# Performance work log

Hardware: AMD Instinct MI355X
Metric: run time of the kernel (lower is better)

## Reference

```python
import jax, jax.numpy as jnp
import numpy as np

N_EMBED = 2048
NUM_EXPERTS = 64
TOP_K = 8
B, S = 4, 8192


def setup_inputs() -> dict:
    key = jax.random.key(0)
    ks = jax.random.split(key, 8)
    scale = 1.0 / np.sqrt(N_EMBED)
    return {
        "x": jax.random.normal(ks[0], (B, S, N_EMBED), dtype=jnp.float32),
        "eps": jax.random.normal(ks[1], (B, S, NUM_EXPERTS), dtype=jnp.float32),
        "w_router": jax.random.uniform(ks[2], (N_EMBED, NUM_EXPERTS), jnp.float32, -scale, scale),
        "b_router": jax.random.uniform(ks[3], (NUM_EXPERTS,), jnp.float32, -scale, scale),
        "w_noise": jax.random.uniform(ks[4], (N_EMBED, NUM_EXPERTS), jnp.float32, -scale, scale),
        "b_noise": jax.random.uniform(ks[5], (NUM_EXPERTS,), jnp.float32, -scale, scale),
        "w_skip": jax.random.uniform(ks[6], (N_EMBED, 1), jnp.float32, -scale, scale),
        "b_skip": jax.random.uniform(ks[7], (1,), jnp.float32, -scale, scale),
    }


def reference(x, eps, w_router, b_router, w_noise, b_noise, w_skip, b_skip):
    # Router and noise logits: [B, S, E]
    logits = jnp.einsum("bsd,de->bse", x, w_router) + b_router
    noise_logits = jnp.einsum("bsd,de->bse", x, w_noise) + b_noise
    # noisy_logits = logits + randn * softplus(noise_logits); randn passed as eps
    noisy_logits = logits + eps * jax.nn.softplus(noise_logits)
    # top-k + scatter(-inf) + softmax == softmax over top-k values scattered back
    top_vals, indices = jax.lax.top_k(noisy_logits, TOP_K)  # [B,S,K]
    gates = jax.nn.softmax(top_vals, axis=-1)  # [B,S,K]
    onehot = jax.nn.one_hot(indices, NUM_EXPERTS, dtype=x.dtype)  # [B,S,K,E]
    router_output = jnp.einsum("bsk,bske->bse", gates, onehot)  # zeros off top-k
    # Sigmoid skip gate: [B, S, 1]
    skip_prob = jax.nn.sigmoid(jnp.einsum("bsd,do->bso", x, w_skip) + b_skip)
    return router_output, indices, skip_prob
```

## Files before the change

kernel.cpp:

```cpp
#include <hip/hip_runtime.h>
#include <math.h>

#define NTOK   32768
#define D      2048
#define E      64
#define TOPK   8

#define BLOCK  256
#define TM     64
#define BK     32
#define NCHUNK (D / BK)
#define NBLK   (NTOK / TM)

#define WBF_BYTES (NCHUNK * 16384)

#define LG_STR 133
#define SP_OFF  34048
#define SMEM_BYTES 34304

#define TIE_EPS 2e-4f

typedef __bf16 bf16x8 __attribute__((ext_vector_type(8)));
typedef float  f32x4  __attribute__((ext_vector_type(4)));

__device__ __forceinline__ unsigned short f2bf_rne(float f) {
    unsigned int u = __float_as_uint(f);
    u += 0x7FFFu + ((u >> 16) & 1u);
    return (unsigned short)(u >> 16);
}

__device__ __forceinline__ void split_pack8(const float* xv, uint4& hv, uint4& lv) {
    unsigned int h[8], l[8];
#pragma unroll
    for (int j = 0; j < 8; ++j) {
        unsigned short hb = f2bf_rne(xv[j]);
        float hf = __uint_as_float(((unsigned int)hb) << 16);
        unsigned short lb = f2bf_rne(xv[j] - hf);
        h[j] = hb; l[j] = lb;
    }
    hv.x = h[0] | (h[1] << 16); hv.y = h[2] | (h[3] << 16);
    hv.z = h[4] | (h[5] << 16); hv.w = h[6] | (h[7] << 16);
    lv.x = l[0] | (l[1] << 16); lv.y = l[2] | (l[3] << 16);
    lv.z = l[4] | (l[5] << 16); lv.w = l[6] | (l[7] << 16);
}

__global__ __launch_bounds__(256) void convert_w_kernel(
    const float* __restrict__ wr, const float* __restrict__ wn, char* __restrict__ wbf)
{
    int u = blockIdx.x * 256 + threadIdx.x;
    int col  = u & 127;
    int koct = (u >> 7) & 3;
    int c    = u >> 9;
    const float* src = (col < 64)
        ? (wr + (size_t)(c * BK + koct * 8) * E + col)
        : (wn + (size_t)(c * BK + koct * 8) * E + (col - 64));
    float xv[8];
#pragma unroll
    for (int j = 0; j < 8; ++j) xv[j] = src[(size_t)j * E];
    uint4 hv, lv;
    split_pack8(xv, hv, lv);
    char* dst = wbf + (size_t)c * 16384 + (size_t)(koct * 128 + col) * 16;
    *(uint4*)dst = hv;
    *(uint4*)(dst + 8192) = lv;
}

__global__ __launch_bounds__(BLOCK, 2) void router_kernel(
    const float* __restrict__ x, const float* __restrict__ eps,
    const char* __restrict__ wbf,
    const float* __restrict__ b_router, const float* __restrict__ b_noise,
    const float* __restrict__ w_skip, const float* __restrict__ b_skip,
    float* __restrict__ out_router, float* __restrict__ out_idx,
    float* __restrict__ out_skip, int* __restrict__ flags, int cap)
{
    __shared__ __attribute__((aligned(16))) char smem[SMEM_BYTES];
    const int tid = threadIdx.x;
    const int tokBase = blockIdx.x * TM;

    const int lane = tid & 63;
    const int wv   = __builtin_amdgcn_readfirstlane(tid >> 6);
    const int tg   = wv >> 1;
    const int ch   = wv & 1;
    const int q    = lane >> 4;
    const int m    = lane & 15;

    const float* xlane = x + (size_t)(tokBase + tg * 32 + m) * D + q * 8;
    const char*  blane = wbf + (size_t)((q << 7) + (ch << 6) + m) * 16;
    const float* wklane = w_skip + q * 8;

    f32x4 acc[2][4];
#pragma unroll
    for (int tt = 0; tt < 2; ++tt)
#pragma unroll
        for (int cw = 0; cw < 4; ++cw) acc[tt][cw] = (f32x4){0.f, 0.f, 0.f, 0.f};
    float skipAcc[2] = {0.f, 0.f};

    struct Gen {
        float4 a[2][2];
        uint4  b[4][2];
        float4 wk[2];
    };

    auto loadGen = [&](Gen& g, int c) {
        const float* xp = xlane + c * BK;
#pragma unroll
        for (int tt = 0; tt < 2; ++tt) {
            g.a[tt][0] = *(const float4*)(xp + (size_t)tt * 16 * D);
            g.a[tt][1] = *(const float4*)(xp + (size_t)tt * 16 * D + 4);
        }
        const char* bp = blane + (size_t)c * 16384;
#pragma unroll
        for (int cw = 0; cw < 4; ++cw) {
            g.b[cw][0] = *(const uint4*)(bp + cw * 256);
            g.b[cw][1] = *(const uint4*)(bp + cw * 256 + 8192);
        }
        g.wk[0] = *(const float4*)(wklane + c * BK);
        g.wk[1] = *(const float4*)(wklane + c * BK + 4);
    };

    auto computeGen = [&](Gen& g) {
#pragma unroll
        for (int tt = 0; tt < 2; ++tt) {
            float xv[8] = {g.a[tt][0].x, g.a[tt][0].y, g.a[tt][0].z, g.a[tt][0].w,
                           g.a[tt][1].x, g.a[tt][1].y, g.a[tt][1].z, g.a[tt][1].w};
            uint4 hv, lv;
            split_pack8(xv, hv, lv);
            bf16x8 Ah = __builtin_bit_cast(bf16x8, hv);
            bf16x8 Al = __builtin_bit_cast(bf16x8, lv);
#pragma unroll
            for (int cw = 0; cw < 4; ++cw) {
                bf16x8 Bh = __builtin_bit_cast(bf16x8, g.b[cw][0]);
                bf16x8 Bl = __builtin_bit_cast(bf16x8, g.b[cw][1]);
                acc[tt][cw] = __builtin_amdgcn_mfma_f32_16x16x32_bf16(Ah, Bh, acc[tt][cw], 0, 0, 0);
                acc[tt][cw] = __builtin_amdgcn_mfma_f32_16x16x32_bf16(Ah, Bl, acc[tt][cw], 0, 0, 0);
                acc[tt][cw] = __builtin_amdgcn_mfma_f32_16x16x32_bf16(Al, Bh, acc[tt][cw], 0, 0, 0);
            }
            float s = skipAcc[tt];
            s = fmaf(xv[0], g.wk[0].x, s); s = fmaf(xv[1], g.wk[0].y, s);
            s = fmaf(xv[2], g.wk[0].z, s); s = fmaf(xv[3], g.wk[0].w, s);
            s = fmaf(xv[4], g.wk[1].x, s); s = fmaf(xv[5], g.wk[1].y, s);
            s = fmaf(xv[6], g.wk[1].z, s); s = fmaf(xv[7], g.wk[1].w, s);
            skipAcc[tt] = s;
        }
    };

    Gen gA, gB;
    loadGen(gA, 0);
#pragma unroll 1
    for (int c = 0; c < NCHUNK; c += 2) {
        loadGen(gB, c + 1);
        computeGen(gA);
        if (c + 2 < NCHUNK) loadGen(gA, c + 2);
        computeGen(gB);
    }

    float* lg = (float*)smem;
#pragma unroll
    for (int tt = 0; tt < 2; ++tt)
#pragma unroll
        for (int cw = 0; cw < 4; ++cw) {
#pragma unroll
            for (int reg = 0; reg < 4; ++reg) {
                int token = tg * 32 + tt * 16 + q * 4 + reg;
                int col = ch * 64 + cw * 16 + m;
                lg[token * LG_STR + col] = acc[tt][cw][reg];
            }
        }

#pragma unroll
    for (int tt = 0; tt < 2; ++tt) {
        skipAcc[tt] += __shfl_xor(skipAcc[tt], 16);
        skipAcc[tt] += __shfl_xor(skipAcc[tt], 32);
    }
    if (ch == 0 && lane < 16) {
        float* sp = (float*)(smem + SP_OFF);
        sp[tg * 32 + lane]      = skipAcc[0];
        sp[tg * 32 + 16 + lane] = skipAcc[1];
    }
    __syncthreads();

    if (tid < 64) {
        const int t = tid;
        const int tok = tokBase + t;
        float* row = lg + t * LG_STR;

        float sv = ((float*)(smem + SP_OFF))[t] + b_skip[0];
        out_skip[tok] = 1.f / (1.f + expf(-sv));

        const float4* epsr = (const float4*)(eps + (size_t)tok * E);
#pragma unroll 4
        for (int e4 = 0; e4 < 16; ++e4) {
            float4 ep = epsr[e4];
            float epv[4] = {ep.x, ep.y, ep.z, ep.w};
#pragma unroll
            for (int u2 = 0; u2 < 4; ++u2) {
                int e = e4 * 4 + u2;
                float lgv = row[e] + b_router[e];
                float nl  = row[64 + e] + b_noise[e];
                float sp  = fmaxf(nl, 0.f) + log1pf(expf(-fabsf(nl)));
                row[e] = lgv + epv[u2] * sp;
            }
        }

        float vals[9];
        int idxs[8];
        for (int p = 0; p < 9; ++p) {
            float best = -INFINITY;
            int bi = 0;
            for (int e = 0; e < 64; ++e) {
                float v = row[e];
                if (v > best) { best = v; bi = e; }
            }
            vals[p] = best;
            if (p < 8) idxs[p] = bi;
            row[bi] = -INFINITY;
        }

        float mg = 1e30f;
#pragma unroll
        for (int p = 0; p < 8; ++p) mg = fminf(mg, vals[p] - vals[p + 1]);
        if (mg < TIE_EPS) {
            int slot = atomicAdd(flags, 1);
            if (slot < cap) flags[2 + slot] = tok;
        }

        float mx = vals[0];
        float g[8], s = 0.f;
#pragma unroll
        for (int p = 0; p < 8; ++p) { g[p] = expf(vals[p] - mx); s += g[p]; }
        float inv = 1.f / s;

        float* rrow = row + 64;
#pragma unroll
        for (int e = 0; e < 64; ++e) rrow[e] = 0.f;
#pragma unroll
        for (int p = 0; p < 8; ++p) rrow[idxs[p]] = g[p] * inv;
#pragma unroll
        for (int e4 = 0; e4 < 16; ++e4) {
            float4 o = make_float4(rrow[e4 * 4], rrow[e4 * 4 + 1],
                                   rrow[e4 * 4 + 2], rrow[e4 * 4 + 3]);
            *(float4*)(out_router + (size_t)tok * E + e4 * 4) = o;
        }
        float4 i0 = make_float4((float)idxs[0], (float)idxs[1], (float)idxs[2], (float)idxs[3]);
        float4 i1 = make_float4((float)idxs[4], (float)idxs[5], (float)idxs[6], (float)idxs[7]);
        *(float4*)(out_idx + (size_t)tok * TOPK)     = i0;
        *(float4*)(out_idx + (size_t)tok * TOPK + 4) = i1;
    }
}

__global__ __launch_bounds__(256) void fixup_kernel(
    const float* __restrict__ x, const float* __restrict__ eps,
    const float* __restrict__ w_router, const float* __restrict__ b_router,
    const float* __restrict__ w_noise, const float* __restrict__ b_noise,
    float* __restrict__ out_router, float* __restrict__ out_idx,
    const int* __restrict__ flags, int cap)
{
    __shared__ double smR[4][64];
    __shared__ double smN[4][64];
    __shared__ double noisy[64];
    const int tid  = threadIdx.x;
    const int lane = tid & 63;
    const int qw   = tid >> 6;

    int count = flags[0];
    if (count > cap) count = cap;

    for (int i = blockIdx.x; i < count; i += gridDim.x) {
        int tok = flags[2 + i];
        const float4* xr4 = (const float4*)(x + (size_t)tok * D + qw * 512);
        const float* wrB = w_router + (size_t)(qw * 512) * E + lane;
        const float* wnB = w_noise  + (size_t)(qw * 512) * E + lane;

        double pr0 = 0, pr1 = 0, pr2 = 0, pr3 = 0;
        double pn0 = 0, pn1 = 0, pn2 = 0, pn3 = 0;
        for (int it = 0; it < 128; ++it) {
            float4 xv = xr4[it];
            const float* wr = wrB + (size_t)(it * 4) * E;
            const float* wn = wnB + (size_t)(it * 4) * E;
            pr0 += (double)xv.x * (double)wr[0];
            pr1 += (double)xv.y * (double)wr[E];
            pr2 += (double)xv.z * (double)wr[2 * E];
            pr3 += (double)xv.w * (double)wr[3 * E];
            pn0 += (double)xv.x * (double)wn[0];
            pn1 += (double)xv.y * (double)wn[E];
            pn2 += (double)xv.z * (double)wn[2 * E];
            pn3 += (double)xv.w * (double)wn[3 * E];
        }
        smR[qw][lane] = (pr0 + pr1) + (pr2 + pr3);
        smN[qw][lane] = (pn0 + pn1) + (pn2 + pn3);
        __syncthreads();

        if (tid < 64) {
            double lgv = smR[0][tid] + smR[1][tid] + smR[2][tid] + smR[3][tid] + (double)b_router[tid];
            double nl  = smN[0][tid] + smN[1][tid] + smN[2][tid] + smN[3][tid] + (double)b_noise[tid];
            double sp  = fmax(nl, 0.0) + log1p(exp(-fabs(nl)));
            noisy[tid] = lgv + (double)eps[(size_t)tok * E + tid] * sp;
        }
        __syncthreads();

        if (tid == 0) {
            double tmp[64];
            for (int j = 0; j < 64; ++j) tmp[j] = noisy[j];
            double vals[8]; int idxs[8];
            for (int p = 0; p < 8; ++p) {
                double best = -1e300; int bi = 0;
                for (int j = 0; j < 64; ++j)
                    if (tmp[j] > best) { best = tmp[j]; bi = j; }
                vals[p] = best; idxs[p] = bi; tmp[bi] = -1e300;
            }
            double mx = vals[0], s = 0.0, g[8];
            for (int p = 0; p < 8; ++p) { g[p] = exp(vals[p] - mx); s += g[p]; }
            float rowv[64];
            for (int j = 0; j < 64; ++j) rowv[j] = 0.f;
            for (int p = 0; p < 8; ++p) rowv[idxs[p]] = (float)(g[p] / s);
            for (int j = 0; j < 64; ++j) out_router[(size_t)tok * E + j] = rowv[j];
            for (int p = 0; p < 8; ++p) out_idx[(size_t)tok * TOPK + p] = (float)idxs[p];
        }
        __syncthreads();
    }
}

extern "C" void kernel_launch(void* const* d_in, const int* in_sizes, int n_in,
                              void* d_out, int out_size, void* d_ws, size_t ws_size,
                              hipStream_t stream) {
    const float* x        = (const float*)d_in[0];
    const float* eps      = (const float*)d_in[1];
    const float* w_router = (const float*)d_in[2];
    const float* b_router = (const float*)d_in[3];
    const float* w_noise  = (const float*)d_in[4];
    const float* b_noise  = (const float*)d_in[5];
    const float* w_skip   = (const float*)d_in[6];
    const float* b_skip   = (const float*)d_in[7];

    float* out = (float*)d_out;
    float* out_router = out;
    float* out_idx    = out + (size_t)NTOK * E;
    float* out_skip   = out_idx + (size_t)NTOK * TOPK;

    char* wbf  = (char*)d_ws;
    int* flags = (int*)((char*)d_ws + WBF_BYTES);
    int cap = 0;
    if (ws_size > WBF_BYTES + 16) {
        size_t c = (ws_size - WBF_BYTES - 8) / 4;
        cap = (c > 16384) ? 16384 : (int)c;
    }

    hipMemsetAsync((char*)d_ws + WBF_BYTES, 0, 8, stream);

    convert_w_kernel<<<dim3(128), dim3(256), 0, stream>>>(w_router, w_noise, wbf);

    router_kernel<<<dim3(NBLK), dim3(BLOCK), 0, stream>>>(
        x, eps, wbf, b_router, b_noise, w_skip, b_skip,
        out_router, out_idx, out_skip, flags, cap);

    fixup_kernel<<<dim3(512), dim3(256), 0, stream>>>(
        x, eps, w_router, b_router, w_noise, b_noise,
        out_router, out_idx, flags, cap);
}
```

Before: 549.9 us.

## Split router GEMM along K into partial-sum kernel plus combine/top-k kernel

```diff
diff --git a/kernel.cpp b/kernel.cpp
--- a/kernel.cpp
+++ b/kernel.cpp
@@ -14,6 +14,13 @@
 
 #define WBF_BYTES (NCHUNK * 16384)
 
+#define FLAGS_OFF   WBF_BYTES
+#define PART_OFF    (WBF_BYTES + 131072)
+#define PART_BYTES  ((size_t)2 * NTOK * 128 * 4)
+#define SKIPP_OFF   (PART_OFF + PART_BYTES)
+#define SKIPP_BYTES ((size_t)2 * NTOK * 4)
+#define WS_NEED     (SKIPP_OFF + SKIPP_BYTES)
+
 #define LG_STR 133
 #define SP_OFF  34048
 #define SMEM_BYTES 34304
@@ -21,6 +28,7 @@
 #define TIE_EPS 2e-4f
 
 typedef __bf16 bf16x8 __attribute__((ext_vector_type(8)));
+typedef __bf16 bf16x2 __attribute__((ext_vector_type(2)));
 typedef float  f32x4  __attribute__((ext_vector_type(4)));
 
 __device__ __forceinline__ unsigned short f2bf_rne(float f) {
@@ -42,6 +50,26 @@
     hv.z = h[4] | (h[5] << 16); hv.w = h[6] | (h[7] << 16);
     lv.x = l[0] | (l[1] << 16); lv.y = l[2] | (l[3] << 16);
     lv.z = l[4] | (l[5] << 16); lv.w = l[6] | (l[7] << 16);
+}
+
+__device__ __forceinline__ unsigned int pk2(float a, float b) {
+    bf16x2 p;
+    p[0] = (__bf16)a; p[1] = (__bf16)b;
+    return __builtin_bit_cast(unsigned int, p);
+}
+__device__ __forceinline__ void split_pack8_v2(const float* xv, uint4& hv, uint4& lv) {
+    unsigned int h[4], l[4];
+#pragma unroll
+    for (int p = 0; p < 4; ++p) {
+        float a = xv[2 * p], b = xv[2 * p + 1];
+        unsigned int hu = pk2(a, b);
+        float fa = __uint_as_float(hu << 16);
+        float fb = __uint_as_float(hu & 0xFFFF0000u);
+        h[p] = hu;
+        l[p] = pk2(a - fa, b - fb);
+    }
+    hv.x = h[0]; hv.y = h[1]; hv.z = h[2]; hv.w = h[3];
+    lv.x = l[0]; lv.y = l[1]; lv.z = l[2]; lv.w = l[3];
 }
 
 __global__ __launch_bounds__(256) void convert_w_kernel(
@@ -62,6 +90,215 @@
     char* dst = wbf + (size_t)c * 16384 + (size_t)(koct * 128 + col) * 16;
     *(uint4*)dst = hv;
     *(uint4*)(dst + 8192) = lv;
+}
+
+__global__ __launch_bounds__(BLOCK, 4) void gemm_part_kernel(
+    const float* __restrict__ x, const char* __restrict__ wbf,
+    const float* __restrict__ w_skip,
+    float* __restrict__ part, float* __restrict__ skip_part)
+{
+    const int tid = threadIdx.x;
+    const int kp  = blockIdx.x & 1;
+    const int tb  = blockIdx.x >> 1;
+    const int tokBase = tb * TM;
+    const int c0 = kp * 32;
+
+    const int lane = tid & 63;
+    const int wv   = __builtin_amdgcn_readfirstlane(tid >> 6);
+    const int tg   = wv >> 1;
+    const int ch   = wv & 1;
+    const int q    = lane >> 4;
+    const int m    = lane & 15;
+
+    const float* xlane  = x + (size_t)(tokBase + tg * 32 + m) * D + q * 8 + (size_t)c0 * BK;
+    const char*  blane  = wbf + (size_t)((q << 7) + (ch << 6) + m) * 16 + (size_t)c0 * 16384;
+    const float* wklane = w_skip + q * 8 + c0 * BK;
+
+    f32x4 acc[2][4];
+#pragma unroll
+    for (int tt = 0; tt < 2; ++tt)
+#pragma unroll
+        for (int cw = 0; cw < 4; ++cw) acc[tt][cw] = (f32x4){0.f, 0.f, 0.f, 0.f};
+    float skipAcc[2] = {0.f, 0.f};
+
+    struct Gen {
+        float4 a[2][2];
+        uint4  b[4][2];
+        float4 wk[2];
+    };
+
+    auto loadGen = [&](Gen& g, int c) {
+        const float* xp = xlane + c * BK;
+#pragma unroll
+        for (int tt = 0; tt < 2; ++tt) {
+            g.a[tt][0] = *(const float4*)(xp + (size_t)tt * 16 * D);
+            g.a[tt][1] = *(const float4*)(xp + (size_t)tt * 16 * D + 4);
+        }
+        const char* bp = blane + (size_t)c * 16384;
+#pragma unroll
+        for (int cw = 0; cw < 4; ++cw) {
+            g.b[cw][0] = *(const uint4*)(bp + cw * 256);
+            g.b[cw][1] = *(const uint4*)(bp + cw * 256 + 8192);
+        }
+        g.wk[0] = *(const float4*)(wklane + c * BK);
+        g.wk[1] = *(const float4*)(wklane + c * BK + 4);
+    };
+
+    auto computeGen = [&](Gen& g) {
+#pragma unroll
+        for (int tt = 0; tt < 2; ++tt) {
+            float xv[8] = {g.a[tt][0].x, g.a[tt][0].y, g.a[tt][0].z, g.a[tt][0].w,
+                           g.a[tt][1].x, g.a[tt][1].y, g.a[tt][1].z, g.a[tt][1].w};
+            uint4 hv, lv;
+            split_pack8_v2(xv, hv, lv);
+            bf16x8 Ah = __builtin_bit_cast(bf16x8, hv);
+            bf16x8 Al = __builtin_bit_cast(bf16x8, lv);
+#pragma unroll
+            for (int cw = 0; cw < 4; ++cw) {
+                bf16x8 Bh = __builtin_bit_cast(bf16x8, g.b[cw][0]);
+                bf16x8 Bl = __builtin_bit_cast(bf16x8, g.b[cw][1]);
+                acc[tt][cw] = __builtin_amdgcn_mfma_f32_16x16x32_bf16(Ah, Bh, acc[tt][cw], 0, 0, 0);
+                acc[tt][cw] = __builtin_amdgcn_mfma_f32_16x16x32_bf16(Ah, Bl, acc[tt][cw], 0, 0, 0);
+                acc[tt][cw] = __builtin_amdgcn_mfma_f32_16x16x32_bf16(Al, Bh, acc[tt][cw], 0, 0, 0);
+            }
+            float s = skipAcc[tt];
+            s = fmaf(xv[0], g.wk[0].x, s); s = fmaf(xv[1], g.wk[0].y, s);
+            s = fmaf(xv[2], g.wk[0].z, s); s = fmaf(xv[3], g.wk[0].w, s);
+            s = fmaf(xv[4], g.wk[1].x, s); s = fmaf(xv[5], g.wk[1].y, s);
+            s = fmaf(xv[6], g.wk[1].z, s); s = fmaf(xv[7], g.wk[1].w, s);
+            skipAcc[tt] = s;
+        }
+    };
+
+    Gen gA, gB;
+    loadGen(gA, 0);
+#pragma unroll 1
+    for (int c = 0; c < 32; c += 2) {
+        loadGen(gB, c + 1);
+        computeGen(gA);
+        if (c + 2 < 32) loadGen(gA, c + 2);
+        computeGen(gB);
+    }
+
+    float* pbase = part + (size_t)kp * NTOK * 128 + (size_t)tokBase * 128;
+#pragma unroll
+    for (int tt = 0; tt < 2; ++tt)
+#pragma unroll
+        for (int cw = 0; cw < 4; ++cw) {
+#pragma unroll
+            for (int reg = 0; reg < 4; ++reg) {
+                int token = tg * 32 + tt * 16 + q * 4 + reg;
+                int col = ch * 64 + cw * 16 + m;
+                pbase[(size_t)token * 128 + col] = acc[tt][cw][reg];
+            }
+        }
+
+#pragma unroll
+    for (int tt = 0; tt < 2; ++tt) {
+        skipAcc[tt] += __shfl_xor(skipAcc[tt], 16);
+        skipAcc[tt] += __shfl_xor(skipAcc[tt], 32);
+    }
+    if (ch == 0 && lane < 16) {
+        float* spg = skip_part + (size_t)kp * NTOK + tokBase + tg * 32;
+        spg[lane]      = skipAcc[0];
+        spg[16 + lane] = skipAcc[1];
+    }
+}
+
+__global__ __launch_bounds__(256) void combine_kernel(
+    const float* __restrict__ part, const float* __restrict__ skip_part,
+    const float* __restrict__ eps,
+    const float* __restrict__ b_router, const float* __restrict__ b_noise,
+    const float* __restrict__ b_skip,
+    float* __restrict__ out_router, float* __restrict__ out_idx,
+    float* __restrict__ out_skip, int* __restrict__ flags, int cap)
+{
+    __shared__ __attribute__((aligned(16))) float lg[TM * LG_STR];
+    const int tid = threadIdx.x;
+    const int blk = blockIdx.x;
+    const int tokBase = blk * TM;
+
+    const float4* p0 = (const float4*)(part + (size_t)blk * TM * 128);
+    const float4* p1 = (const float4*)(part + (size_t)NTOK * 128 + (size_t)blk * TM * 128);
+#pragma unroll
+    for (int r = 0; r < 8; ++r) {
+        int j = r * 256 + tid;
+        float4 a = p0[j], b = p1[j];
+        int tok = j >> 5;
+        int col = (j & 31) * 4;
+        float* dst = lg + tok * LG_STR + col;
+        dst[0] = a.x + b.x; dst[1] = a.y + b.y;
+        dst[2] = a.z + b.z; dst[3] = a.w + b.w;
+    }
+    __syncthreads();
+
+    if (tid < 64) {
+        const int t = tid;
+        const int tok = tokBase + t;
+        float* row = lg + t * LG_STR;
+
+        float sv = skip_part[tok] + skip_part[NTOK + tok] + b_skip[0];
+        out_skip[tok] = 1.f / (1.f + expf(-sv));
+
+        const float4* epsr = (const float4*)(eps + (size_t)tok * E);
+#pragma unroll 4
+        for (int e4 = 0; e4 < 16; ++e4) {
+            float4 ep = epsr[e4];
+            float epv[4] = {ep.x, ep.y, ep.z, ep.w};
+#pragma unroll
+            for (int u2 = 0; u2 < 4; ++u2) {
+                int e = e4 * 4 + u2;
+                float lgv = row[e] + b_router[e];
+                float nl  = row[64 + e] + b_noise[e];
+                float sp  = fmaxf(nl, 0.f) + log1pf(expf(-fabsf(nl)));
+                row[e] = lgv + epv[u2] * sp;
+            }
+        }
+
+        float vals[9];
+        int idxs[8];
+        for (int p = 0; p < 9; ++p) {
+            float best = -INFINITY;
+            int bi = 0;
+            for (int e = 0; e < 64; ++e) {
+                float v = row[e];
+                if (v > best) { best = v; bi = e; }
+            }
+            vals[p] = best;
+            if (p < 8) idxs[p] = bi;
+            row[bi] = -INFINITY;
+        }
+
+        float mg = 1e30f;
+#pragma unroll
+        for (int p = 0; p < 8; ++p) mg = fminf(mg, vals[p] - vals[p + 1]);
+        if (mg < TIE_EPS) {
+            int slot = atomicAdd(flags, 1);
+            if (slot < cap) flags[2 + slot] = tok;
+        }
+
+        float mx = vals[0];
+        float g[8], s = 0.f;
+#pragma unroll
+        for (int p = 0; p < 8; ++p) { g[p] = expf(vals[p] - mx); s += g[p]; }
+        float inv = 1.f / s;
+
+        float* rrow = row + 64;
+#pragma unroll
+        for (int e = 0; e < 64; ++e) rrow[e] = 0.f;
+#pragma unroll
+        for (int p = 0; p < 8; ++p) rrow[idxs[p]] = g[p] * inv;
+#pragma unroll
+        for (int e4 = 0; e4 < 16; ++e4) {
+            float4 o = make_float4(rrow[e4 * 4], rrow[e4 * 4 + 1],
+                                   rrow[e4 * 4 + 2], rrow[e4 * 4 + 3]);
+            *(float4*)(out_router + (size_t)tok * E + e4 * 4) = o;
+        }
+        float4 i0 = make_float4((float)idxs[0], (float)idxs[1], (float)idxs[2], (float)idxs[3]);
+        float4 i1 = make_float4((float)idxs[4], (float)idxs[5], (float)idxs[6], (float)idxs[7]);
+        *(float4*)(out_idx + (size_t)tok * TOPK)     = i0;
+        *(float4*)(out_idx + (size_t)tok * TOPK + 4) = i1;
+    }
 }
 
 __global__ __launch_bounds__(BLOCK, 2) void router_kernel(
@@ -337,22 +574,41 @@
     float* out_skip   = out_idx + (size_t)NTOK * TOPK;
 
     char* wbf  = (char*)d_ws;
-    int* flags = (int*)((char*)d_ws + WBF_BYTES);
-    int cap = 0;
-    if (ws_size > WBF_BYTES + 16) {
-        size_t c = (ws_size - WBF_BYTES - 8) / 4;
-        cap = (c > 16384) ? 16384 : (int)c;
-    }
-
-    hipMemsetAsync((char*)d_ws + WBF_BYTES, 0, 8, stream);
+    int* flags = (int*)((char*)d_ws + FLAGS_OFF);
 
     convert_w_kernel<<<dim3(128), dim3(256), 0, stream>>>(w_router, w_noise, wbf);
 
-    router_kernel<<<dim3(NBLK), dim3(BLOCK), 0, stream>>>(
-        x, eps, wbf, b_router, b_noise, w_skip, b_skip,
-        out_router, out_idx, out_skip, flags, cap);
-
-    fixup_kernel<<<dim3(512), dim3(256), 0, stream>>>(
-        x, eps, w_router, b_router, w_noise, b_noise,
-        out_router, out_idx, flags, cap);
-}
+    if (ws_size >= WS_NEED) {
+        int cap = 16384;
+        hipMemsetAsync((char*)d_ws + FLAGS_OFF, 0, 8, stream);
+
+        float* part      = (float*)((char*)d_ws + PART_OFF);
+        float* skip_part = (float*)((char*)d_ws + SKIPP_OFF);
+
+        gemm_part_kernel<<<dim3(2 * NBLK), dim3(BLOCK), 0, stream>>>(
+            x, wbf, w_skip, part, skip_part);
+
+        combine_kernel<<<dim3(NBLK), dim3(BLOCK), 0, stream>>>(
+            part, skip_part, eps, b_router, b_noise, b_skip,
+            out_router, out_idx, out_skip, flags, cap);
+
+        fixup_kernel<<<dim3(512), dim3(256), 0, stream>>>(
+            x, eps, w_router, b_router, w_noise, b_noise,
+            out_router, out_idx, flags, cap);
+    } else {
+        int cap = 0;
+        if (ws_size > WBF_BYTES + 16) {
+            size_t c = (ws_size - WBF_BYTES - 8) / 4;
+            cap = (c > 16384) ? 16384 : (int)c;
+        }
+        hipMemsetAsync((char*)d_ws + FLAGS_OFF, 0, 8, stream);
+
+        router_kernel<<<dim3(NBLK), dim3(BLOCK), 0, stream>>>(
+            x, eps, wbf, b_router, b_noise, w_skip, b_skip,
+            out_router, out_idx, out_skip, flags, cap);
+
+        fixup_kernel<<<dim3(512), dim3(256), 0, stream>>>(
+            x, eps, w_router, b_router, w_noise, b_noise,
+            out_router, out_idx, flags, cap);
+    }
+}
```

After: 880.3 us. 60.1% more time.
